# Performance work log

Measured on AMD Instinct MI355X. Metric: run time of the kernel, lower is better.

The kernel has to match this reference:

```python
import jax, jax.numpy as jnp
import numpy as np

N_EXPERTS = 8
TOP_K = 2


def setup_inputs() -> dict:
    key = jax.random.key(0)
    k1, k2, k3, k4 = jax.random.split(key, 4)
    B, T, C, H, E = 2, 2048, 1024, 4096, N_EXPERTS
    x = jax.random.normal(k1, (B, T, C), dtype=jnp.float32)
    # weights scaled like standard init to keep activations well-behaved
    router_w = jax.random.normal(k2, (E, C), dtype=jnp.float32) * 0.02
    w1 = jax.random.normal(k3, (E, C, H), dtype=jnp.float32) * (1.0 / np.sqrt(C))
    w2 = jax.random.normal(k4, (E, H, C), dtype=jnp.float32) * (1.0 / np.sqrt(H))
    return {"x": x, "router_w": router_w, "w1": w1, "w2": w2}


def reference(x, router_w, w1, w2):
    B, T, C = x.shape
    E = N_EXPERTS
    xf = x.reshape(-1, C)                                   # [N, C], N = B*T
    logits = jnp.einsum('nc,ec->ne', xf, router_w)          # router (no bias)
    probs = jax.nn.softmax(logits, axis=-1)
    top_w, top_i = jax.lax.top_k(probs, TOP_K)              # [N, K]
    top_w = top_w / jnp.sum(top_w, axis=-1, keepdims=True)  # renormalize
    # combine weight per (token, expert): sum of top-k weights routed to e
    comb = jnp.einsum('nk,nke->ne', top_w, jax.nn.one_hot(top_i, E, dtype=xf.dtype))
    # dense all-expert compute (bias=False, exact GELU, dropout=0 at eval)
    h = jax.nn.gelu(jnp.einsum('nc,ech->enh', xf, w1), approximate=False)  # [E, N, H]
    y = jnp.einsum('enh,ehc->enc', h, w2)                   # [E, N, C]
    out = jnp.einsum('ne,enc->nc', comb, y)                 # weighted combine
    return out.reshape(B, T, C)
```

## Files before the change

kernel.cpp:

```cpp
#include <hip/hip_runtime.h>
#include <hip/hip_bf16.h>
#include <stdint.h>

#define NTOK 4096
#define CD   1024
#define HD   4096
#define NE   8

typedef __attribute__((ext_vector_type(8))) short bf16x8;
typedef __attribute__((ext_vector_type(4))) float f32x4;
typedef __attribute__((ext_vector_type(4))) unsigned short us4;

__device__ __forceinline__ unsigned short f2bf(float f){
  __hip_bfloat16 h = __float2bfloat16(f);
  return *reinterpret_cast<unsigned short*>(&h);
}

__global__ __launch_bounds__(256) void router_kernel(
    const float* __restrict__ x, const float* __restrict__ rw,
    unsigned short* __restrict__ x_bf, int* __restrict__ top_i,
    float* __restrict__ top_w, int* __restrict__ counts){
  __shared__ float rw_lds[NE*CD];
  int tid = threadIdx.x;
  for (int i = tid; i < NE*CD/4; i += 256)
    ((float4*)rw_lds)[i] = ((const float4*)rw)[i];
  __syncthreads();
  int l = tid & 63, w = tid >> 6;
  int n = blockIdx.x*4 + w;

  float4 xv[4];
  #pragma unroll
  for (int j = 0; j < 4; ++j)
    xv[j] = ((const float4*)(x + (size_t)n*CD))[l + j*64];

  #pragma unroll
  for (int j = 0; j < 4; ++j){
    us4 o; o.x = f2bf(xv[j].x); o.y = f2bf(xv[j].y); o.z = f2bf(xv[j].z); o.w = f2bf(xv[j].w);
    *(us4*)(x_bf + (size_t)n*CD + l*4 + j*256) = o;
  }

  double le[NE];
  #pragma unroll
  for (int e = 0; e < NE; ++e){
    double p = 0.0;
    #pragma unroll
    for (int j = 0; j < 4; ++j){
      float4 rv = ((const float4*)(rw_lds + e*CD))[l + j*64];
      p += (double)xv[j].x*rv.x + (double)xv[j].y*rv.y + (double)xv[j].z*rv.z + (double)xv[j].w*rv.w;
    }
    #pragma unroll
    for (int d = 32; d >= 1; d >>= 1) p += __shfl_xor(p, d);
    le[e] = p;
  }
  if (l == 0){
    double m = le[0];
    #pragma unroll
    for (int e = 1; e < NE; ++e) m = le[e] > m ? le[e] : m;
    double pe[NE], s = 0.0;
    #pragma unroll
    for (int e = 0; e < NE; ++e){ pe[e] = exp(le[e]-m); s += pe[e]; }
    (void)s;
    int i0 = 0;
    #pragma unroll
    for (int e = 1; e < NE; ++e) if (pe[e] > pe[i0]) i0 = e;
    int i1 = (i0 == 0) ? 1 : 0;
    #pragma unroll
    for (int e = 0; e < NE; ++e){ if (e == i0) continue; if (pe[e] > pe[i1]) i1 = e; }
    double w0 = pe[i0], w1v = pe[i1], wsum = w0 + w1v;
    top_i[2*n] = i0; top_i[2*n+1] = i1;
    top_w[2*n] = (float)(w0/wsum); top_w[2*n+1] = (float)(w1v/wsum);
    atomicAdd(&counts[i0], 1); atomicAdd(&counts[i1], 1);
  }
}

__global__ void scan_kernel(const int* __restrict__ counts, int* __restrict__ offsets, int* __restrict__ cursor){
  if (threadIdx.x == 0){
    int s = 0;
    for (int e = 0; e < NE; ++e){ offsets[e] = s; cursor[e] = s; s += counts[e]; }
  }
}

__global__ __launch_bounds__(256) void scatter_kernel(
    const int* __restrict__ top_i, const float* __restrict__ top_w,
    int* __restrict__ cursor, int* __restrict__ g_tok, float* __restrict__ g_w){
  int n = blockIdx.x*256 + threadIdx.x;
  #pragma unroll
  for (int k = 0; k < 2; ++k){
    int e = top_i[2*n+k];
    int pos = atomicAdd(&cursor[e], 1);
    g_tok[pos] = n;
    g_w[pos] = top_w[2*n+k];
  }
}

template<int R, int S>
__global__ __launch_bounds__(256) void transpose_cvt(const float* __restrict__ in, unsigned short* __restrict__ outp){
  __shared__ float tile[64][65];
  int e = blockIdx.z;
  const float* ip = in + (size_t)e*R*S;
  unsigned short* op = outp + (size_t)e*R*S;
  int s0 = blockIdx.x*64, r0 = blockIdx.y*64;
  int tid = threadIdx.x;
  #pragma unroll
  for (int i = 0; i < 4; ++i){
    int lin = i*256 + tid;
    int rr = lin >> 4, c4 = lin & 15;
    float4 v = *(const float4*)(ip + (size_t)(r0+rr)*S + s0 + c4*4);
    tile[rr][c4*4+0] = v.x; tile[rr][c4*4+1] = v.y;
    tile[rr][c4*4+2] = v.z; tile[rr][c4*4+3] = v.w;
  }
  __syncthreads();
  #pragma unroll
  for (int i = 0; i < 4; ++i){
    int lin = i*256 + tid;
    int ss = lin >> 4, rq = lin & 15;
    us4 o;
    o.x = f2bf(tile[rq*4+0][ss]);
    o.y = f2bf(tile[rq*4+1][ss]);
    o.z = f2bf(tile[rq*4+2][ss]);
    o.w = f2bf(tile[rq*4+3][ss]);
    *(us4*)(op + (size_t)(s0+ss)*R + r0 + rq*4) = o;
  }
}

template<int KLEN, int SPLITK, int EPI>
__global__ __launch_bounds__(512, 2) void gemm256(
    const unsigned short* __restrict__ A_src,
    const unsigned short* __restrict__ B_src,
    unsigned short* __restrict__ h_out,
    float* __restrict__ outp,
    const int* __restrict__ g_tok,
    const float* __restrict__ g_w,
    const int* __restrict__ counts,
    const int* __restrict__ offsets,
    int NDIM, int KSTRIDE){
  constexpr int NT = KLEN/64;
  __shared__ alignas(128) char lds[131072];

  int z = blockIdx.z;
  int e  = (SPLITK == 1) ? z : (z / SPLITK);
  int kz = (SPLITK == 1) ? 0 : (z % SPLITK);
  int n_e = counts[e];
  int m0 = blockIdx.y*256;
  if (m0 >= n_e) return;
  int n0 = blockIdx.x*256;
  int g_base = offsets[e];
  int kstart = kz*KLEN;

  int tid = threadIdx.x, l = tid & 63, w = tid >> 6;
  int wr = w >> 2, wc = w & 3;
  int lrow = l & 15, q = l >> 4;

  const unsigned short* src[8];
  uint32_t dst[8];
  #pragma unroll
  for (int i = 0; i < 8; ++i){
    int s = w*4 + (i & 3);
    bool isA = i < 4;
    int row = s*8 + (l >> 3);
    int chunk = (l & 7) ^ (row & 7);
    if (isA){
      int rg = m0 + row; if (rg > n_e-1) rg = n_e-1;
      size_t arow;
      if (EPI == 0) arow = (size_t)g_tok[g_base + rg];
      else          arow = (size_t)(g_base + rg);
      src[i] = A_src + arow*(size_t)KSTRIDE + kstart + chunk*8;
    } else {
      src[i] = B_src + ((size_t)e*NDIM + n0 + row)*(size_t)KSTRIDE + kstart + chunk*8;
    }
    dst[i] = (isA ? 0u : 32768u) + (uint32_t)s*1024u;
  }

  uint32_t a_off[8], b_off[4];
  #pragma unroll
  for (int m = 0; m < 8; ++m){
    int ra = wr*128 + m*16 + lrow;
    a_off[m] = ra*128 + 16*(q ^ (ra & 7));
  }
  #pragma unroll
  for (int n = 0; n < 4; ++n){
    int rb = wc*64 + n*16 + lrow;
    b_off[n] = 32768u + rb*128 + 16*(q ^ (rb & 7));
  }

  f32x4 acc[8][4] = {};

  #pragma unroll
  for (int i = 0; i < 8; ++i){
    __builtin_amdgcn_global_load_lds((const __attribute__((address_space(1))) void*)src[i],
                                     (__attribute__((address_space(3))) void*)&lds[dst[i]], 16, 0, 0);
    src[i] += 64;
  }
  __syncthreads();

  uint32_t buf = 0;
  for (int kt = 0; kt < NT; ++kt){
    if (kt + 1 < NT){
      uint32_t nb = (buf ^ 1)*65536u;
      #pragma unroll
      for (int i = 0; i < 8; ++i){
        __builtin_amdgcn_global_load_lds((const __attribute__((address_space(1))) void*)src[i],
                                         (__attribute__((address_space(3))) void*)&lds[dst[i] + nb], 16, 0, 0);
        src[i] += 64;
      }
    }
    uint32_t ro = buf*65536u;
    #pragma unroll
    for (int ks = 0; ks < 2; ++ks){
      bf16x8 av[8], bv[4];
      #pragma unroll
      for (int m = 0; m < 8; ++m)
        av[m] = *(const bf16x8*)&lds[(a_off[m] ^ (ks*64)) + ro];
      #pragma unroll
      for (int n = 0; n < 4; ++n)
        bv[n] = *(const bf16x8*)&lds[(b_off[n] ^ (ks*64)) + ro];
      __builtin_amdgcn_s_setprio(1);
      #pragma unroll
      for (int m = 0; m < 8; ++m)
        #pragma unroll
        for (int n = 0; n < 4; ++n)
          acc[m][n] = __builtin_amdgcn_mfma_f32_16x16x32_bf16(av[m], bv[n], acc[m][n], 0, 0, 0);
      __builtin_amdgcn_s_setprio(0);
    }
    __syncthreads();
    buf ^= 1;
  }

  if (EPI == 0){
    #pragma unroll
    for (int m = 0; m < 8; ++m){
      #pragma unroll
      for (int j = 0; j < 4; ++j){
        int r = m0 + wr*128 + m*16 + q*4 + j;
        if (r < n_e){
          unsigned short* hp = h_out + (size_t)(g_base + r)*NDIM + n0 + wc*64 + lrow;
          #pragma unroll
          for (int n = 0; n < 4; ++n){
            float v = acc[m][n][j];
            v = 0.5f*v*(1.0f + erff(v*0.70710678118654752f));
            hp[n*16] = f2bf(v);
          }
        }
      }
    }
  } else {
    #pragma unroll
    for (int m = 0; m < 8; ++m){
      #pragma unroll
      for (int j = 0; j < 4; ++j){
        int r = m0 + wr*128 + m*16 + q*4 + j;
        if (r < n_e){
          int slot = g_base + r;
          int t = g_tok[slot];
          float wgt = g_w[slot];
          float* op = outp + (size_t)t*NDIM + n0 + wc*64 + lrow;
          #pragma unroll
          for (int n = 0; n < 4; ++n)
            atomicAdd(op + n*16, wgt*acc[m][n][j]);
        }
      }
    }
  }
}

extern "C" void kernel_launch(void* const* d_in, const int* in_sizes, int n_in,
                              void* d_out, int out_size, void* d_ws, size_t ws_size,
                              hipStream_t stream) {
  const float* x  = (const float*)d_in[0];
  const float* rw = (const float*)d_in[1];
  const float* w1 = (const float*)d_in[2];
  const float* w2 = (const float*)d_in[3];

  size_t off = 0;
  auto alloc = [&](size_t sz) -> char* {
    char* p = (char*)d_ws + off;
    off += (sz + 255) & ~(size_t)255;
    return p;
  };
  unsigned short* x_bf = (unsigned short*)alloc((size_t)NTOK*CD*2);
  unsigned short* w1t  = (unsigned short*)alloc((size_t)NE*CD*HD*2);
  unsigned short* w2t  = (unsigned short*)alloc((size_t)NE*CD*HD*2);
  unsigned short* hbuf = (unsigned short*)alloc((size_t)NTOK*2*HD*2);
  int*   top_i  = (int*)alloc(NTOK*2*4);
  float* top_w  = (float*)alloc(NTOK*2*4);
  int*   counts = (int*)alloc(64);
  int*   offs   = (int*)alloc(64);
  int*   cursor = (int*)alloc(64);
  int*   g_tok  = (int*)alloc(NTOK*2*4);
  float* g_w    = (float*)alloc(NTOK*2*4);
  (void)ws_size; (void)in_sizes; (void)n_in; (void)out_size;

  hipMemsetAsync(d_out, 0, (size_t)NTOK*CD*4, stream);
  hipMemsetAsync(counts, 0, 64, stream);

  router_kernel<<<dim3(NTOK/4), dim3(256), 0, stream>>>(x, rw, x_bf, top_i, top_w, counts);
  scan_kernel<<<dim3(1), dim3(64), 0, stream>>>(counts, offs, cursor);
  scatter_kernel<<<dim3(NTOK/256), dim3(256), 0, stream>>>(top_i, top_w, cursor, g_tok, g_w);

  transpose_cvt<CD, HD><<<dim3(HD/64, CD/64, NE), dim3(256), 0, stream>>>(w1, w1t);
  transpose_cvt<HD, CD><<<dim3(CD/64, HD/64, NE), dim3(256), 0, stream>>>(w2, w2t);

  gemm256<CD, 1, 0><<<dim3(HD/256, 8, NE), dim3(512), 0, stream>>>(
      x_bf, w1t, hbuf, (float*)nullptr, g_tok, g_w, counts, offs, HD, CD);
  gemm256<HD/2, 2, 1><<<dim3(CD/256, 8, NE*2), dim3(512), 0, stream>>>(
      hbuf, w2t, (unsigned short*)nullptr, (float*)d_out, g_tok, g_w, counts, offs, CD, HD);
}
```

Baseline: 509.3 us.

## Rewrite expert GEMM as 8-phase pipelined kernel with split-half staging

Replaces the double-buffered GEMM loop with an 8-phase schedule that splits the A and B tiles into halves. Each half's global-to-LDS load is interleaved with LDS reads and MFMA blocks, using explicit s_barrier and vmcnt waits. This is meant to overlap memory traffic with compute more finely than one full-tile prefetch per iteration. It also raises the grid y dimension to 16 for more token-tile coverage, raises the second GEMM's split-K from 2 to 4, and drops an unused softmax sum in the router. The hand-written waitcnt and barrier sequencing is fragile, and the larger split-K adds more atomic output traffic.

```diff
diff --git a/kernel.cpp b/kernel.cpp
--- a/kernel.cpp
+++ b/kernel.cpp
@@ -10,6 +10,10 @@
 typedef __attribute__((ext_vector_type(8))) short bf16x8;
 typedef __attribute__((ext_vector_type(4))) float f32x4;
 typedef __attribute__((ext_vector_type(4))) unsigned short us4;
+
+#define BARR() asm volatile("s_barrier" ::: "memory")
+#define VMW4() asm volatile("s_waitcnt vmcnt(4)" ::: "memory")
+#define VMW0() asm volatile("s_waitcnt vmcnt(0)" ::: "memory")
 
 __device__ __forceinline__ unsigned short f2bf(float f){
   __hip_bfloat16 h = __float2bfloat16(f);
@@ -56,10 +60,9 @@
     double m = le[0];
     #pragma unroll
     for (int e = 1; e < NE; ++e) m = le[e] > m ? le[e] : m;
-    double pe[NE], s = 0.0;
-    #pragma unroll
-    for (int e = 0; e < NE; ++e){ pe[e] = exp(le[e]-m); s += pe[e]; }
-    (void)s;
+    double pe[NE];
+    #pragma unroll
+    for (int e = 0; e < NE; ++e) pe[e] = exp(le[e]-m);
     int i0 = 0;
     #pragma unroll
     for (int e = 1; e < NE; ++e) if (pe[e] > pe[i0]) i0 = e;
@@ -123,8 +126,8 @@
   }
 }
 
-template<int KLEN, int SPLITK, int EPI>
-__global__ __launch_bounds__(512, 2) void gemm256(
+template<int EPI, int SPLITK>
+__global__ __launch_bounds__(512, 2) void gemm8ph(
     const unsigned short* __restrict__ A_src,
     const unsigned short* __restrict__ B_src,
     unsigned short* __restrict__ h_out,
@@ -134,97 +137,123 @@
     const int* __restrict__ counts,
     const int* __restrict__ offsets,
     int NDIM, int KSTRIDE){
-  constexpr int NT = KLEN/64;
   __shared__ alignas(128) char lds[131072];
 
   int z = blockIdx.z;
-  int e  = (SPLITK == 1) ? z : (z / SPLITK);
-  int kz = (SPLITK == 1) ? 0 : (z % SPLITK);
+  int e  = z / SPLITK;
+  int kz = z % SPLITK;
   int n_e = counts[e];
   int m0 = blockIdx.y*256;
   if (m0 >= n_e) return;
   int n0 = blockIdx.x*256;
   int g_base = offsets[e];
-  int kstart = kz*KLEN;
+  int kstart = kz*1024;
 
   int tid = threadIdx.x, l = tid & 63, w = tid >> 6;
   int wr = w >> 2, wc = w & 3;
   int lrow = l & 15, q = l >> 4;
 
-  const unsigned short* src[8];
-  uint32_t dst[8];
-  #pragma unroll
-  for (int i = 0; i < 8; ++i){
-    int s = w*4 + (i & 3);
-    bool isA = i < 4;
-    int row = s*8 + (l >> 3);
-    int chunk = (l & 7) ^ (row & 7);
-    if (isA){
-      int rg = m0 + row; if (rg > n_e-1) rg = n_e-1;
-      size_t arow;
-      if (EPI == 0) arow = (size_t)g_tok[g_base + rg];
-      else          arow = (size_t)(g_base + rg);
-      src[i] = A_src + arow*(size_t)KSTRIDE + kstart + chunk*8;
-    } else {
-      src[i] = B_src + ((size_t)e*NDIM + n0 + row)*(size_t)KSTRIDE + kstart + chunk*8;
-    }
-    dst[i] = (isA ? 0u : 32768u) + (uint32_t)s*1024u;
-  }
-
-  uint32_t a_off[8], b_off[4];
-  #pragma unroll
-  for (int m = 0; m < 8; ++m){
-    int ra = wr*128 + m*16 + lrow;
-    a_off[m] = ra*128 + 16*(q ^ (ra & 7));
-  }
-  #pragma unroll
-  for (int n = 0; n < 4; ++n){
-    int rb = wc*64 + n*16 + lrow;
-    b_off[n] = 32768u + rb*128 + 16*(q ^ (rb & 7));
-  }
-
-  f32x4 acc[8][4] = {};
-
-  #pragma unroll
-  for (int i = 0; i < 8; ++i){
-    __builtin_amdgcn_global_load_lds((const __attribute__((address_space(1))) void*)src[i],
-                                     (__attribute__((address_space(3))) void*)&lds[dst[i]], 16, 0, 0);
-    src[i] += 64;
-  }
-  __syncthreads();
-
-  uint32_t buf = 0;
-  for (int kt = 0; kt < NT; ++kt){
-    if (kt + 1 < NT){
-      uint32_t nb = (buf ^ 1)*65536u;
-      #pragma unroll
-      for (int i = 0; i < 8; ++i){
-        __builtin_amdgcn_global_load_lds((const __attribute__((address_space(1))) void*)src[i],
-                                         (__attribute__((address_space(3))) void*)&lds[dst[i] + nb], 16, 0, 0);
-        src[i] += 64;
+  const unsigned short* sp[4][2];
+  uint32_t sd[4][2];
+  #pragma unroll
+  for (int kind = 0; kind < 4; ++kind){
+    #pragma unroll
+    for (int j = 0; j < 2; ++j){
+      int r = j*64 + w*8 + (l >> 3);
+      int h = kind >> 1;
+      int c = (l & 7) ^ (r & 7);
+      if ((kind & 1) == 0){
+        int trow = (r >> 6)*128 + h*64 + (r & 63);
+        int rg = m0 + trow; if (rg > n_e-1) rg = n_e-1;
+        size_t arow = (EPI == 0) ? (size_t)g_tok[g_base + rg] : (size_t)(g_base + rg);
+        sp[kind][j] = A_src + arow*(size_t)KSTRIDE + kstart + c*8;
+        sd[kind][j] = h*16384u + (uint32_t)(j*8192 + w*1024 + l*16);
+      } else {
+        int trow = (r >> 5)*64 + h*32 + (r & 31);
+        sp[kind][j] = B_src + ((size_t)e*NDIM + n0 + trow)*(size_t)KSTRIDE + kstart + c*8;
+        sd[kind][j] = 32768u + h*16384u + (uint32_t)(j*8192 + w*1024 + l*16);
       }
     }
-    uint32_t ro = buf*65536u;
-    #pragma unroll
-    for (int ks = 0; ks < 2; ++ks){
-      bf16x8 av[8], bv[4];
-      #pragma unroll
-      for (int m = 0; m < 8; ++m)
-        av[m] = *(const bf16x8*)&lds[(a_off[m] ^ (ks*64)) + ro];
-      #pragma unroll
-      for (int n = 0; n < 4; ++n)
-        bv[n] = *(const bf16x8*)&lds[(b_off[n] ^ (ks*64)) + ro];
-      __builtin_amdgcn_s_setprio(1);
-      #pragma unroll
-      for (int m = 0; m < 8; ++m)
+  }
+
+  auto STG = [&](int kind, int buf, int kt){
+    #pragma unroll
+    for (int j = 0; j < 2; ++j)
+      __builtin_amdgcn_global_load_lds(
+        (const __attribute__((address_space(1))) void*)(sp[kind][j] + kt*64),
+        (__attribute__((address_space(3))) void*)&lds[sd[kind][j] + (uint32_t)buf*65536u], 16, 0, 0);
+  };
+
+  uint32_t aoff[2][4], boff[2][2];
+  #pragma unroll
+  for (int mh = 0; mh < 2; ++mh)
+    #pragma unroll
+    for (int mm = 0; mm < 4; ++mm)
+      aoff[mh][mm] = mh*16384u + (uint32_t)((wr*64 + mm*16 + lrow)*128) + 16u*(q ^ (lrow & 7));
+  #pragma unroll
+  for (int nh = 0; nh < 2; ++nh)
+    #pragma unroll
+    for (int nn = 0; nn < 2; ++nn)
+      boff[nh][nn] = 32768u + nh*16384u + (uint32_t)((wc*32 + nn*16 + lrow)*128) + 16u*(q ^ (lrow & 7));
+
+  bf16x8 a[4][2], b[2][2][2];
+  f32x4 acc[8][4] = {};
+
+  auto RDA = [&](int mh, int buf){
+    #pragma unroll
+    for (int mm = 0; mm < 4; ++mm)
+      #pragma unroll
+      for (int ks = 0; ks < 2; ++ks)
+        a[mm][ks] = *(const bf16x8*)&lds[(aoff[mh][mm] ^ (ks*64)) + (uint32_t)buf*65536u];
+  };
+  auto RDB = [&](int nh, int buf){
+    #pragma unroll
+    for (int nn = 0; nn < 2; ++nn)
+      #pragma unroll
+      for (int ks = 0; ks < 2; ++ks)
+        b[nh][nn][ks] = *(const bf16x8*)&lds[(boff[nh][nn] ^ (ks*64)) + (uint32_t)buf*65536u];
+  };
+  auto MM = [&](int mh, int nh){
+    __builtin_amdgcn_s_setprio(1);
+    #pragma unroll
+    for (int mm = 0; mm < 4; ++mm)
+      #pragma unroll
+      for (int nn = 0; nn < 2; ++nn)
         #pragma unroll
-        for (int n = 0; n < 4; ++n)
-          acc[m][n] = __builtin_amdgcn_mfma_f32_16x16x32_bf16(av[m], bv[n], acc[m][n], 0, 0, 0);
-      __builtin_amdgcn_s_setprio(0);
-    }
-    __syncthreads();
-    buf ^= 1;
-  }
+        for (int ks = 0; ks < 2; ++ks)
+          acc[mh*4+mm][nh*2+nn] =
+            __builtin_amdgcn_mfma_f32_16x16x32_bf16(a[mm][ks], b[nh][nn][ks], acc[mh*4+mm][nh*2+nn], 0, 0, 0);
+    __builtin_amdgcn_s_setprio(0);
+  };
+
+  STG(0,0,0); STG(1,0,0); STG(2,0,0); STG(3,0,0);
+  STG(0,1,1); STG(1,1,1);
+  VMW4();
+  BARR();
+
+  auto iter = [&](int i, bool last){
+    int t1 = 2*i + 1;
+    RDA(0,0); RDB(0,0); STG(2,1,t1);
+    BARR(); MM(0,0); BARR();
+    RDB(1,0); STG(3,1,t1);
+    BARR(); MM(0,1); BARR();
+    RDA(1,0); if (!last) STG(0,0,t1+1);
+    BARR(); MM(1,0); BARR();
+    if (!last){ STG(1,0,t1+1); VMW4(); } else { VMW0(); }
+    BARR(); MM(1,1); BARR();
+    RDA(0,1); RDB(0,1); if (!last) STG(2,0,t1+1);
+    BARR(); MM(0,0); BARR();
+    RDB(1,1); if (!last) STG(3,0,t1+1);
+    BARR(); MM(0,1); BARR();
+    RDA(1,1); if (!last) STG(0,1,t1+2);
+    BARR(); MM(1,0); BARR();
+    if (!last){ STG(1,1,t1+2); VMW4(); }
+    BARR(); MM(1,1); BARR();
+  };
+
+  #pragma unroll 1
+  for (int i = 0; i < 7; ++i) iter(i, false);
+  iter(7, true);
 
   if (EPI == 0){
     #pragma unroll
@@ -300,8 +329,8 @@
   transpose_cvt<CD, HD><<<dim3(HD/64, CD/64, NE), dim3(256), 0, stream>>>(w1, w1t);
   transpose_cvt<HD, CD><<<dim3(CD/64, HD/64, NE), dim3(256), 0, stream>>>(w2, w2t);
 
-  gemm256<CD, 1, 0><<<dim3(HD/256, 8, NE), dim3(512), 0, stream>>>(
+  gemm8ph<0, 1><<<dim3(16, 16, NE), dim3(512), 0, stream>>>(
       x_bf, w1t, hbuf, (float*)nullptr, g_tok, g_w, counts, offs, HD, CD);
-  gemm256<HD/2, 2, 1><<<dim3(CD/256, 8, NE*2), dim3(512), 0, stream>>>(
+  gemm8ph<1, 4><<<dim3(4, 16, NE*4), dim3(512), 0, stream>>>(
       hbuf, w2t, (unsigned short*)nullptr, (float*)d_out, g_tok, g_w, counts, offs, CD, HD);
 }
```

Measured after the change: 613.3 us. 1.2x slower.
